# Performance work log

Hardware: AMD Instinct MI355X
Metric: run time of the kernel (lower is better)

The kernel has to match this reference:

```python
import jax, jax.numpy as jnp
import numpy as np

EPS = 1e-5
NUM_HEADS = 8
KEY_CH = 512
VAL_CH = 512


def instance_norm(x):
    # x: [B, N, C]; torch InstanceNorm1d normalizes over the length dim (N) per (b, c), no affine
    m = jnp.mean(x, axis=1, keepdims=True)
    v = jnp.var(x, axis=1, keepdims=True)
    return (x - m) / jnp.sqrt(v + EPS)


def setup_inputs() -> dict:
    key = jax.random.key(0)
    ks = jax.random.split(key, 16)
    B, HW, D, NL, LC = 8, 16384, 512, 20, 768
    s = 0.02
    inp = {
        "x": jax.random.normal(ks[0], (B, HW, D), dtype=jnp.float32),
        "l": jax.random.normal(ks[1], (B, NL, LC), dtype=jnp.float32),
        "l_mask": jnp.ones((B, NL), dtype=jnp.float32),
        # vis_project conv1d(dim->dim)
        "Wv": jax.random.normal(ks[2], (D, D), dtype=jnp.float32) * s,
        "bv": jnp.zeros((D,), dtype=jnp.float32),
        # f_query conv1d(v_in->key)
        "Wq": jax.random.normal(ks[3], (D, KEY_CH), dtype=jnp.float32) * s,
        "bq": jnp.zeros((KEY_CH,), dtype=jnp.float32),
        # f_key conv1d(l_in->key)
        "Wk": jax.random.normal(ks[4], (LC, KEY_CH), dtype=jnp.float32) * s,
        "bk": jnp.zeros((KEY_CH,), dtype=jnp.float32),
        # f_value conv1d(l_in->value)
        "Wval": jax.random.normal(ks[5], (LC, VAL_CH), dtype=jnp.float32) * s,
        "bval": jnp.zeros((VAL_CH,), dtype=jnp.float32),
        # W conv1d(value->out)
        "Ww": jax.random.normal(ks[6], (VAL_CH, VAL_CH), dtype=jnp.float32) * s,
        "bw": jnp.zeros((VAL_CH,), dtype=jnp.float32),
        # project_mm conv1d(value->value)
        "Wm": jax.random.normal(ks[7], (VAL_CH, VAL_CH), dtype=jnp.float32) * s,
        "bm": jnp.zeros((VAL_CH,), dtype=jnp.float32),
    }
    return inp


def reference(x, l, l_mask, Wv, bv, Wq, bq, Wk, bk, Wval, bval, Ww, bw, Wm, bm):
    B, HW, _ = x.shape
    n_l = l.shape[1]
    H = NUM_HEADS
    dk = KEY_CH // H
    dv = VAL_CH // H

    # vis_project: 1x1 conv + GELU (exact) + dropout(p=0)
    vis = jax.nn.gelu(x @ Wv + bv, approximate=False)  # [B, HW, D]

    # SpatialImageLanguageAttention
    q = instance_norm(x @ Wq + bq)          # [B, HW, Kc], InstanceNorm over HW
    k = l @ Wk + bk                          # [B, n_l, Kc]
    v = l @ Wval + bval                      # [B, n_l, Vc]

    q = q.reshape(B, HW, H, dk)              # bqhd
    k = k.reshape(B, n_l, H, dk)             # bkhd
    v = v.reshape(B, n_l, H, dv)             # bkhd

    sim = jnp.einsum("bqhd,bkhd->bhqk", q, k) * (KEY_CH ** -0.5)
    sim = jax.nn.softmax(sim, axis=-1)       # softmax over short language seq
    out = jnp.einsum("bhqk,bkhd->bqhd", sim, v).reshape(B, HW, VAL_CH)

    lang = instance_norm(out @ Ww + bw)      # [B, HW, Vc]

    # gated fusion + project_mm
    mm = vis * lang
    mm = jax.nn.gelu(mm @ Wm + bm, approximate=False)
    return mm
```

## Files before the change

### kernel.cpp

```cpp
#include <hip/hip_runtime.h>

#define HWN 16384
#define DMODEL 512
#define NLANG 20
#define LCH 768
#define NB 8
#define MTOT (NB*HWN)
#define NHEADS 8

typedef float floatx4 __attribute__((ext_vector_type(4)));
typedef short short8 __attribute__((ext_vector_type(8)));

__device__ __forceinline__ float bflo(unsigned u){ return __uint_as_float(u << 16); }
__device__ __forceinline__ float bfhi(unsigned u){ return __uint_as_float(u & 0xffff0000u); }
__device__ __forceinline__ unsigned short f2bf(float f){
  unsigned u = __float_as_uint(f);
  u += 0x7fffu + ((u >> 16) & 1u);
  return (unsigned short)(u >> 16);
}
__device__ __forceinline__ unsigned pack2(float a, float b){
  return (unsigned)f2bf(a) | ((unsigned)f2bf(b) << 16);
}
__device__ __forceinline__ float geluf(float v){
  float t = v * v;
  float u2 = v * fmaf(t, -0.0713548162f, -1.5957691216f);
  float e = __expf(u2);
  return v * __builtin_amdgcn_rcpf(1.0f + e);
}
__device__ __forceinline__ void stage16(const void* g, void* l){
  __builtin_amdgcn_global_load_lds(
      (const __attribute__((address_space(1))) void*)g,
      (__attribute__((address_space(3))) void*)l, 16, 0, 0);
}
__device__ __forceinline__ int tslot(int c){ return ((c & 7) << 3) | (c >> 3); }

template<int CTRL>
__device__ __forceinline__ float dppf(float x){
  return __int_as_float(__builtin_amdgcn_mov_dpp(__float_as_int(x), CTRL, 0xf, 0xf, true));
}
__device__ __forceinline__ void quadT(float v[4], int lane){
  float t0 = dppf<0xB1>(v[1]), t1 = dppf<0xB1>(v[0]);
  float t2 = dppf<0xB1>(v[3]), t3 = dppf<0xB1>(v[2]);
  int p0 = lane & 1;
  float w0 = (p0 == 0) ? v[0] : t0;
  float w1 = (p0 == 1) ? v[1] : t1;
  float w2 = (p0 == 0) ? v[2] : t2;
  float w3 = (p0 == 1) ? v[3] : t3;
  float s0 = dppf<0x4E>(w2), s1 = dppf<0x4E>(w3);
  float s2 = dppf<0x4E>(w0), s3 = dppf<0x4E>(w1);
  int p1 = lane & 2;
  v[0] = (p1 == 0) ? w0 : s0;
  v[1] = (p1 == 0) ? w1 : s1;
  v[2] = (p1 == 2) ? w2 : s2;
  v[3] = (p1 == 2) ? w3 : s3;
}

__global__ void prep_w(const float* __restrict__ Wv, const float* __restrict__ Wq,
                       const float* __restrict__ Wm,
                       unsigned short* __restrict__ wcatT, unsigned short* __restrict__ wmT)
{
  int i = blockIdx.x * 256 + threadIdx.x;
  if (i < 1024 * 512) {
    int n = i >> 9, k = i & 511;
    float v = (n < 512) ? Wv[k * 512 + n] : Wq[k * 512 + (n - 512)];
    wcatT[i] = f2bf(v);
  } else {
    int j = i - 1024 * 512;
    int n = j >> 9, k = j & 511;
    wmT[j] = f2bf(Wm[k * 512 + n]);
  }
}

__global__ void xcvt(const float* __restrict__ x, unsigned short* __restrict__ xb)
{
  size_t i = ((size_t)blockIdx.x * 256 + threadIdx.x) * 8;
  float4 a = *reinterpret_cast<const float4*>(&x[i]);
  float4 b = *reinterpret_cast<const float4*>(&x[i + 4]);
  uint4 d;
  d.x = pack2(a.x, a.y); d.y = pack2(a.z, a.w);
  d.z = pack2(b.x, b.y); d.w = pack2(b.z, b.w);
  *reinterpret_cast<uint4*>(&xb[i]) = d;
}

__global__ void mmk(const unsigned short* __restrict__ y, const unsigned short* __restrict__ vis,
                    const float* __restrict__ lma, const float* __restrict__ lmb,
                    unsigned short* __restrict__ mm)
{
  size_t i = ((size_t)blockIdx.x * 256 + threadIdx.x) * 8;
  int c = (int)(i & 511);
  int b = (int)(i >> 23);
  uint4 yv = *reinterpret_cast<const uint4*>(&y[i]);
  uint4 vv = *reinterpret_cast<const uint4*>(&vis[i]);
  const float* Ap = &lma[b * 512 + c];
  const float* Bp = &lmb[b * 512 + c];
  float4 a0 = *reinterpret_cast<const float4*>(Ap);
  float4 a1 = *reinterpret_cast<const float4*>(Ap + 4);
  float4 b0 = *reinterpret_cast<const float4*>(Bp);
  float4 b1 = *reinterpret_cast<const float4*>(Bp + 4);
  float m0 = bflo(vv.x) * (bflo(yv.x) * a0.x + b0.x);
  float m1 = bfhi(vv.x) * (bfhi(yv.x) * a0.y + b0.y);
  float m2 = bflo(vv.y) * (bflo(yv.y) * a0.z + b0.z);
  float m3 = bfhi(vv.y) * (bfhi(yv.y) * a0.w + b0.w);
  float m4 = bflo(vv.z) * (bflo(yv.z) * a1.x + b1.x);
  float m5 = bfhi(vv.z) * (bfhi(yv.z) * a1.y + b1.y);
  float m6 = bflo(vv.w) * (bflo(yv.w) * a1.z + b1.z);
  float m7 = bfhi(vv.w) * (bfhi(yv.w) * a1.w + b1.w);
  uint4 d;
  d.x = pack2(m0, m1); d.y = pack2(m2, m3);
  d.z = pack2(m4, m5); d.w = pack2(m6, m7);
  *reinterpret_cast<uint4*>(&mm[i]) = d;
}

__global__ void prep_kv(const float* __restrict__ l, const float* __restrict__ Wk,
                        const float* __restrict__ bk, const float* __restrict__ Wval,
                        const float* __restrict__ bval,
                        float* __restrict__ kraw, unsigned short* __restrict__ vb)
{
  int i = blockIdx.x * 256 + threadIdx.x;
  int which = i / (NB * NLANG * 512);
  int j = i - which * (NB * NLANG * 512);
  int bt = j >> 9;
  int c = j & 511;
  const float* W = which ? Wval : Wk;
  float acc = which ? bval[c] : bk[c];
  const float* lr = l + (size_t)bt * LCH;
  for (int p = 0; p < LCH; p++) acc = fmaf(lr[p], W[p * 512 + c], acc);
  if (which) vb[j] = f2bf(acc);
  else       kraw[j] = acc;
}

__global__ void w2prep(const unsigned short* __restrict__ vb, const float* __restrict__ Ww,
                       unsigned short* __restrict__ w2t)
{
  int i = blockIdx.x * 256 + threadIdx.x;
  int k = i & 255;
  int n = (i >> 8) & 511;
  int b = i >> 17;
  int t = k & 31, h = k >> 5;
  float acc = 0.f;
  if (t < NLANG) {
    const unsigned short* vr = &vb[(size_t)(b * NLANG + t) * 512 + h * 64];
    const float* wr = &Ww[(size_t)(h * 64) * 512 + n];
    #pragma unroll 8
    for (int d = 0; d < 64; d++)
      acc = fmaf(__uint_as_float((unsigned)vr[d] << 16), wr[d * 512], acc);
  }
  w2t[(size_t)(b * 512 + n) * 256 + k] = f2bf(acc);
}

__global__ void kprep(const float* __restrict__ qsum, const float* __restrict__ qsq,
                      const float* __restrict__ kraw, unsigned short* __restrict__ kp,
                      float* __restrict__ offG)
{
  int blk = blockIdx.x; int b = blk / NLANG, t = blk - b * NLANG;
  int lane = threadIdx.x;
  float offp = 0.f;
  float vals[8];
  #pragma unroll
  for (int e = 0; e < 8; e++) {
    int c = lane * 8 + e;
    float mean = qsum[b * 512 + c] * (1.f / 16384.f);
    float var  = qsq[b * 512 + c] * (1.f / 16384.f) - mean * mean;
    float inv  = rsqrtf(var + 1e-5f);
    float a = inv * 0.044194173824159216f;
    float kv = kraw[((size_t)(b * NLANG + t)) * 512 + c];
    vals[e] = kv * a;
    offp += (-mean * a) * kv;
  }
  unsigned u0 = pack2(vals[0], vals[1]);
  unsigned u1 = pack2(vals[2], vals[3]);
  unsigned u2 = pack2(vals[4], vals[5]);
  unsigned u3 = pack2(vals[6], vals[7]);
  uint4 uu = make_uint4(u0, u1, u2, u3);
  *reinterpret_cast<uint4*>(&kp[((size_t)(b * NLANG + t)) * 512 + tslot(lane) * 8]) = uu;
  offp += __shfl_xor(offp, 1);
  offp += __shfl_xor(offp, 2);
  offp += __shfl_xor(offp, 4);
  if ((lane & 7) == 0) offG[(b * 8 + (lane >> 3)) * NLANG + t] = offp;
}

__global__ void lmk(const float* __restrict__ ysum, const float* __restrict__ ysq,
                    float* __restrict__ lma, float* __restrict__ lmb)
{
  int i = blockIdx.x * 256 + threadIdx.x;
  if (i < NB * 512) {
    float mean = ysum[i] * (1.f / 16384.f);
    float var  = ysq[i] * (1.f / 16384.f) - mean * mean;
    float inv  = rsqrtf(var + 1e-5f);
    lma[i] = inv; lmb[i] = -mean * inv;
  }
}

__global__ __launch_bounds__(256, 3) void attn_k(
    const unsigned short* __restrict__ kp, const float* __restrict__ offG,
    const unsigned short* __restrict__ qb, unsigned short* __restrict__ pb)
{
  __shared__ __align__(16) unsigned short kps[NLANG * 512];
  __shared__ __align__(16) unsigned short qs[32 * 512];
  __shared__ float offs[NHEADS * NLANG];
  int tid = threadIdx.x, bid = blockIdx.x;
  int b = bid >> 9;
  int row0 = (bid & 511) * 32;
  size_t base = (size_t)b * (NLANG * 512);
  const uint4* kg = reinterpret_cast<const uint4*>(kp + base);
  uint4* kl = reinterpret_cast<uint4*>(kps);
  #pragma unroll
  for (int i = 0; i < 5; i++) { int o = i * 256 + tid; kl[o] = kg[o]; }
  if (tid < NHEADS * NLANG) offs[tid] = offG[b * (NHEADS * NLANG) + tid];

  size_t grow0 = (size_t)b * HWN + row0;
  #pragma unroll
  for (int i = 0; i < 8; i++) {
    int g = i * 256 + tid;
    int row = g >> 6, c = g & 63;
    uint4 d = *reinterpret_cast<const uint4*>(&qb[(grow0 + row) * 512 + c * 8]);
    *reinterpret_cast<uint4*>(&qs[row * 512 + tslot(c) * 8]) = d;
  }
  __syncthreads();

  int r = tid >> 3, h = tid & 7;
  float sim[NLANG];
  #pragma unroll
  for (int t = 0; t < NLANG; t++) sim[t] = offs[h * NLANG + t];
  #pragma unroll
  for (int j = 0; j < 8; j++) {
    uint4 qv = *reinterpret_cast<const uint4*>(&qs[r * 512 + (j * 8 + h) * 8]);
    float q0 = bflo(qv.x), q1 = bfhi(qv.x), q2 = bflo(qv.y), q3 = bfhi(qv.y);
    float q4 = bflo(qv.z), q5 = bfhi(qv.z), q6 = bflo(qv.w), q7 = bfhi(qv.w);
    #pragma unroll
    for (int t = 0; t < NLANG; t++) {
      uint4 kv = *reinterpret_cast<const uint4*>(&kps[t * 512 + (j * 8 + h) * 8]);
      float a = sim[t];
      a = fmaf(q0, bflo(kv.x), a); a = fmaf(q1, bfhi(kv.x), a);
      a = fmaf(q2, bflo(kv.y), a); a = fmaf(q3, bfhi(kv.y), a);
      a = fmaf(q4, bflo(kv.z), a); a = fmaf(q5, bfhi(kv.z), a);
      a = fmaf(q6, bflo(kv.w), a); a = fmaf(q7, bfhi(kv.w), a);
      sim[t] = a;
    }
  }
  float mx = sim[0];
  #pragma unroll
  for (int t = 1; t < NLANG; t++) mx = fmaxf(mx, sim[t]);
  float s = 0.f;
  #pragma unroll
  for (int t = 0; t < NLANG; t++) { float e = __expf(sim[t] - mx); sim[t] = e; s += e; }
  float invs = 1.f / s;
  #pragma unroll
  for (int t = 0; t < NLANG; t++) sim[t] *= invs;

  unsigned uu[16];
  #pragma unroll
  for (int j = 0; j < 10; j++) uu[j] = pack2(sim[2 * j], sim[2 * j + 1]);
  #pragma unroll
  for (int j = 10; j < 16; j++) uu[j] = 0u;
  size_t prow = (grow0 + r) * 256 + h * 32;
  #pragma unroll
  for (int j = 0; j < 4; j++)
    *reinterpret_cast<uint4*>(&pb[prow + j * 8]) =
        make_uint4(uu[4 * j], uu[4 * j + 1], uu[4 * j + 2], uu[4 * j + 3]);
}

template<int MODE, int KD>
__global__ __launch_bounds__(256) void gemm_k(
    const unsigned short* __restrict__ A,
    const unsigned short* __restrict__ Bw,
    const float* __restrict__ bias0, const float* __restrict__ bias1,
    unsigned short* __restrict__ Out0, unsigned short* __restrict__ Out1,
    float* __restrict__ OutF,
    float* __restrict__ sum1, float* __restrict__ sum2)
{
  constexpr int GN  = (MODE == 0) ? 8 : 4;
  constexpr int NWG = (MODE == 0) ? 8192 : 4096;
  constexpr int KT  = KD / 32;
  constexpr int CS  = 136;
  __shared__ __align__(16) unsigned short SM[6 * 128 * 32];

  int raw = blockIdx.x;
  int lid = (raw & 7) * (NWG / 8) + (raw >> 3);
  int tileN = lid & (GN - 1);
  int tileM = lid / GN;
  int tm128 = tileM * 128;
  int b512 = (tileM >> 7) * 512;
  int tid = threadIdx.x;
  int wave = tid >> 6, lane = tid & 63;
  int wr = (wave >> 1) * 64, wc = (wave & 1) * 64;
  int r15 = lane & 15, kcg = lane >> 4;

  floatx4 acc[4][4];
  floatx4 zz = {0.f, 0.f, 0.f, 0.f};
  #pragma unroll
  for (int m = 0; m < 4; m++)
    #pragma unroll
    for (int n = 0; n < 4; n++) acc[m][n] = zz;

  const unsigned short* Arow = A + (size_t)tm128 * KD;
  const unsigned short* Brow = Bw +
      ((MODE == 1) ? (size_t)(tileM >> 7) * 512 * KD : (size_t)0) +
      (size_t)(tileN * 128) * KD;

  auto stage = [&](int kt, int s) {
    int k0 = kt * 32;
    unsigned short* As = SM + s * 4096;
    unsigned short* Bs = SM + (3 + s) * 4096;
    #pragma unroll
    for (int i = 0; i < 2; i++) {
      int idx = i * 256 + tid;
      int row = idx >> 2;
      int c = (idx & 3) ^ ((row >> 1) & 3);
      stage16(&Arow[(size_t)row * KD + k0 + c * 8],
              &As[(i * 256 + wave * 64) * 8]);
    }
    #pragma unroll
    for (int i = 0; i < 2; i++) {
      int idx = i * 256 + tid;
      int row = idx >> 2;
      int c = (idx & 3) ^ ((row >> 1) & 3);
      stage16(&Brow[(size_t)row * KD + k0 + c * 8],
              &Bs[(i * 256 + wave * 64) * 8]);
    }
  };

  stage(0, 0);
  stage(1, 1);
  #pragma unroll
  for (int kt = 0; kt < KT; kt++) {
    int s = kt % 3;
    __builtin_amdgcn_sched_barrier(0);
    if (kt < KT - 1) asm volatile("s_waitcnt vmcnt(4) lgkmcnt(0)\n\ts_barrier" ::: "memory");
    else             asm volatile("s_waitcnt vmcnt(0) lgkmcnt(0)\n\ts_barrier" ::: "memory");
    __builtin_amdgcn_sched_barrier(0);
    if (kt + 2 < KT) stage(kt + 2, (kt + 2) % 3);
    const unsigned short* As = SM + s * 4096;
    const unsigned short* Bs = SM + (3 + s) * 4096;
    short8 af[4], bfv[4];
    #pragma unroll
    for (int m = 0; m < 4; m++) {
      int R = wr + m * 16 + r15;
      af[m] = *reinterpret_cast<const short8*>(&As[R * 32 + (kcg ^ ((R >> 1) & 3)) * 8]);
    }
    #pragma unroll
    for (int n = 0; n < 4; n++) {
      int R = wc + n * 16 + r15;
      bfv[n] = *reinterpret_cast<const short8*>(&Bs[R * 32 + (kcg ^ ((R >> 1) & 3)) * 8]);
    }
    #pragma unroll
    for (int m = 0; m < 4; m++)
      #pragma unroll
      for (int n = 0; n < 4; n++)
        acc[m][n] = __builtin_amdgcn_mfma_f32_16x16x32_bf16(af[m], bfv[n], acc[m][n], 0, 0, 0);
  }

  if constexpr (MODE != 2) __syncthreads();

  int rowTl = wr + (lane >> 4) * 4 + (lane & 3);
  int c4Tl  = wc + ((lane >> 2) & 3) * 4;

  if constexpr (MODE == 2) {
    #pragma unroll
    for (int n = 0; n < 4; n++) {
      int gcol = tileN * 128 + wc + n * 16 + r15;
      #pragma unroll
      for (int m = 0; m < 4; m++) {
        float v[4];
        #pragma unroll
        for (int j = 0; j < 4; j++) v[j] = geluf(acc[m][n][j] + bias0[gcol]);
        quadT(v, lane);
        int grow = tm128 + m * 16 + rowTl;
        int gc4  = tileN * 128 + n * 16 + c4Tl;
        float4 f4; f4.x = v[0]; f4.y = v[1]; f4.z = v[2]; f4.w = v[3];
        *reinterpret_cast<float4*>(&OutF[(size_t)grow * 512 + gc4]) = f4;
      }
    }
  } else {
    unsigned short* C = SM;
    #pragma unroll
    for (int n = 0; n < 4; n++) {
      int gcol = tileN * 128 + wc + n * 16 + r15;
      float s1 = 0.f, s2 = 0.f;
      #pragma unroll
      for (int m = 0; m < 4; m++) {
        float v[4];
        #pragma unroll
        for (int j = 0; j < 4; j++) v[j] = acc[m][n][j];
        if constexpr (MODE == 0) {
          if (tileN < 4) {
            #pragma unroll
            for (int j = 0; j < 4; j++) v[j] = geluf(v[j] + bias0[gcol]);
          } else {
            #pragma unroll
            for (int j = 0; j < 4; j++) { v[j] += bias1[gcol - 512]; s1 += v[j]; s2 += v[j] * v[j]; }
          }
        } else {
          #pragma unroll
          for (int j = 0; j < 4; j++) { v[j] += bias0[gcol]; s1 += v[j]; s2 += v[j] * v[j]; }
        }
        quadT(v, lane);
        int lrow = m * 16 + rowTl;
        int lc4  = n * 16 + c4Tl;
        uint2 d2; d2.x = pack2(v[0], v[1]); d2.y = pack2(v[2], v[3]);
        *reinterpret_cast<uint2*>(&C[lrow * CS + lc4]) = d2;
      }
      bool doStats = (MODE == 1) || (tileN >= 4);
      if (doStats) {
        s1 += __shfl_xor(s1, 16); s1 += __shfl_xor(s1, 32);
        s2 += __shfl_xor(s2, 16); s2 += __shfl_xor(s2, 32);
        if (lane < 16) {
          int c = (MODE == 0) ? (gcol - 512) : gcol;
          atomicAdd(&sum1[b512 + c], s1);
          atomicAdd(&sum2[b512 + c], s2);
        }
      }
    }
    __syncthreads();
    unsigned short* Og;
    int colbase;
    if constexpr (MODE == 0) {
      if (tileN < 4) { Og = Out0; colbase = tileN * 128; }
      else           { Og = Out1; colbase = (tileN - 4) * 128; }
    } else {
      Og = Out0; colbase = tileN * 128;
    }
    #pragma unroll
    for (int t = 0; t < 8; t++) {
      int cid = t * 256 + tid;
      int row = cid >> 4, cc = cid & 15;
      uint4 d = *reinterpret_cast<const uint4*>(&C[row * CS + cc * 8]);
      *reinterpret_cast<uint4*>(&Og[(size_t)(tm128 + row) * 512 + colbase + cc * 8]) = d;
    }
  }
}

extern "C" void kernel_launch(void* const* d_in, const int* in_sizes, int n_in,
                              void* d_out, int out_size, void* d_ws, size_t ws_size,
                              hipStream_t stream)
{
  const float* x   = (const float*)d_in[0];
  const float* l   = (const float*)d_in[1];
  const float* Wv  = (const float*)d_in[3];
  const float* bv  = (const float*)d_in[4];
  const float* Wq  = (const float*)d_in[5];
  const float* bq  = (const float*)d_in[6];
  const float* Wk  = (const float*)d_in[7];
  const float* bk  = (const float*)d_in[8];
  const float* Wva = (const float*)d_in[9];
  const float* bva = (const float*)d_in[10];
  const float* Ww  = (const float*)d_in[11];
  const float* bw  = (const float*)d_in[12];
  const float* Wm  = (const float*)d_in[13];
  const float* bm  = (const float*)d_in[14];

  char* w = (char*)d_ws;
  size_t o = 0;
  auto alloc = [&](size_t bytes) { size_t r = o; o += (bytes + 255) & ~(size_t)255; return r; };
  size_t WCATT = alloc(1024 * 512 * 2);
  size_t WMT   = alloc(512 * 512 * 2);
  size_t W2T   = alloc((size_t)NB * 512 * 256 * 2);
  size_t KRAW  = alloc((size_t)NB * NLANG * 512 * 4);
  size_t VB    = alloc((size_t)NB * NLANG * 512 * 2);
  size_t KP    = alloc((size_t)NB * NLANG * 512 * 2);
  size_t OFFW  = alloc((size_t)NB * NHEADS * NLANG * 4);
  size_t STATS = alloc((size_t)4 * NB * 512 * 4);
  size_t LMA   = alloc((size_t)NB * 512 * 4);
  size_t LMB   = alloc((size_t)NB * 512 * 4);
  size_t XB    = alloc((size_t)MTOT * 512 * 2);
  size_t VIS   = alloc((size_t)MTOT * 512 * 2);
  size_t QBUF  = alloc((size_t)MTOT * 512 * 2);
  size_t PB    = alloc((size_t)MTOT * 256 * 2);
  size_t YBUF  = alloc((size_t)MTOT * 512 * 2);

  float* qsum = (float*)(w + STATS);
  float* qsq  = qsum + NB * 512;
  float* ysum = qsq + NB * 512;
  float* ysq  = ysum + NB * 512;

  hipMemsetAsync(w + STATS, 0, (size_t)4 * NB * 512 * 4, stream);
  prep_w<<<3072, 256, 0, stream>>>(Wv, Wq, Wm,
      (unsigned short*)(w + WCATT), (unsigned short*)(w + WMT));
  xcvt<<<32768, 256, 0, stream>>>(x, (unsigned short*)(w + XB));
  prep_kv<<<640, 256, 0, stream>>>(l, Wk, bk, Wva, bva,
      (float*)(w + KRAW), (unsigned short*)(w + VB));
  w2prep<<<4096, 256, 0, stream>>>((const unsigned short*)(w + VB), Ww,
      (unsigned short*)(w + W2T));
  gemm_k<0, 512><<<8192, 256, 0, stream>>>((const unsigned short*)(w + XB),
      (const unsigned short*)(w + WCATT), bv, bq,
      (unsigned short*)(w + VIS), (unsigned short*)(w + QBUF), nullptr, qsum, qsq);
  kprep<<<160, 64, 0, stream>>>(qsum, qsq, (const float*)(w + KRAW),
      (unsigned short*)(w + KP), (float*)(w + OFFW));
  attn_k<<<4096, 256, 0, stream>>>((const unsigned short*)(w + KP),
      (const float*)(w + OFFW), (const unsigned short*)(w + QBUF),
      (unsigned short*)(w + PB));
  gemm_k<1, 256><<<4096, 256, 0, stream>>>((const unsigned short*)(w + PB),
      (const unsigned short*)(w + W2T), bw, nullptr,
      (unsigned short*)(w + YBUF), nullptr, nullptr, ysum, ysq);
  lmk<<<16, 256, 0, stream>>>(ysum, ysq, (float*)(w + LMA), (float*)(w + LMB));
  mmk<<<32768, 256, 0, stream>>>((const unsigned short*)(w + YBUF),
      (const unsigned short*)(w + VIS), (const float*)(w + LMA), (const float*)(w + LMB),
      (unsigned short*)(w + XB));
  gemm_k<2, 512><<<4096, 256, 0, stream>>>((const unsigned short*)(w + XB),
      (const unsigned short*)(w + WMT), bm, nullptr,
      nullptr, nullptr, (float*)d_out, nullptr, nullptr);
}
```

Measured before the change: 803.3 us.

## Fuse fp32->bf16 conversion and gating multiply into GEMM A-operand staging

Removes the standalone xcvt and mmk elementwise kernels. The first GEMM now loads fp32 x through registers and converts it to bf16 before writing LDS. The last GEMM reads Y and VIS directly and applies the instance-norm affine and gating multiply while staging its A tile. This saves several full-size HBM round trips, around a gigabyte of traffic, at the cost of register-staged A loads and extra VGPR pressure in the GEMM pipeline. Each block also redundantly re-reads A across its N tiles.

```diff
diff --git a/kernel.cpp b/kernel.cpp
--- a/kernel.cpp
+++ b/kernel.cpp
@@ -71,46 +71,6 @@
   }
 }
 
-__global__ void xcvt(const float* __restrict__ x, unsigned short* __restrict__ xb)
-{
-  size_t i = ((size_t)blockIdx.x * 256 + threadIdx.x) * 8;
-  float4 a = *reinterpret_cast<const float4*>(&x[i]);
-  float4 b = *reinterpret_cast<const float4*>(&x[i + 4]);
-  uint4 d;
-  d.x = pack2(a.x, a.y); d.y = pack2(a.z, a.w);
-  d.z = pack2(b.x, b.y); d.w = pack2(b.z, b.w);
-  *reinterpret_cast<uint4*>(&xb[i]) = d;
-}
-
-__global__ void mmk(const unsigned short* __restrict__ y, const unsigned short* __restrict__ vis,
-                    const float* __restrict__ lma, const float* __restrict__ lmb,
-                    unsigned short* __restrict__ mm)
-{
-  size_t i = ((size_t)blockIdx.x * 256 + threadIdx.x) * 8;
-  int c = (int)(i & 511);
-  int b = (int)(i >> 23);
-  uint4 yv = *reinterpret_cast<const uint4*>(&y[i]);
-  uint4 vv = *reinterpret_cast<const uint4*>(&vis[i]);
-  const float* Ap = &lma[b * 512 + c];
-  const float* Bp = &lmb[b * 512 + c];
-  float4 a0 = *reinterpret_cast<const float4*>(Ap);
-  float4 a1 = *reinterpret_cast<const float4*>(Ap + 4);
-  float4 b0 = *reinterpret_cast<const float4*>(Bp);
-  float4 b1 = *reinterpret_cast<const float4*>(Bp + 4);
-  float m0 = bflo(vv.x) * (bflo(yv.x) * a0.x + b0.x);
-  float m1 = bfhi(vv.x) * (bfhi(yv.x) * a0.y + b0.y);
-  float m2 = bflo(vv.y) * (bflo(yv.y) * a0.z + b0.z);
-  float m3 = bfhi(vv.y) * (bfhi(yv.y) * a0.w + b0.w);
-  float m4 = bflo(vv.z) * (bflo(yv.z) * a1.x + b1.x);
-  float m5 = bfhi(vv.z) * (bfhi(yv.z) * a1.y + b1.y);
-  float m6 = bflo(vv.w) * (bflo(yv.w) * a1.z + b1.z);
-  float m7 = bfhi(vv.w) * (bfhi(yv.w) * a1.w + b1.w);
-  uint4 d;
-  d.x = pack2(m0, m1); d.y = pack2(m2, m3);
-  d.z = pack2(m4, m5); d.w = pack2(m6, m7);
-  *reinterpret_cast<uint4*>(&mm[i]) = d;
-}
-
 __global__ void prep_kv(const float* __restrict__ l, const float* __restrict__ Wk,
                         const float* __restrict__ bk, const float* __restrict__ Wval,
                         const float* __restrict__ bval,
@@ -262,7 +222,9 @@
 
 template<int MODE, int KD>
 __global__ __launch_bounds__(256) void gemm_k(
-    const unsigned short* __restrict__ A,
+    const void* __restrict__ Ag,
+    const unsigned short* __restrict__ Vis,
+    const float* __restrict__ lmA, const float* __restrict__ lmB,
     const unsigned short* __restrict__ Bw,
     const float* __restrict__ bias0, const float* __restrict__ bias1,
     unsigned short* __restrict__ Out0, unsigned short* __restrict__ Out1,
@@ -273,7 +235,9 @@
   constexpr int NWG = (MODE == 0) ? 8192 : 4096;
   constexpr int KT  = KD / 32;
   constexpr int CS  = 136;
-  __shared__ __align__(16) unsigned short SM[6 * 128 * 32];
+  constexpr bool REGA = (MODE != 1);
+  __shared__ __align__(16) unsigned short SM[6 * 4096 + 2048];
+  float* CO = reinterpret_cast<float*>(SM + 6 * 4096);
 
   int raw = blockIdx.x;
   int lid = (raw & 7) * (NWG / 8) + (raw >> 3);
@@ -293,43 +257,122 @@
     #pragma unroll
     for (int n = 0; n < 4; n++) acc[m][n] = zz;
 
-  const unsigned short* Arow = A + (size_t)tm128 * KD;
+  const float* ArowF = nullptr;
+  const unsigned short* ArowS = nullptr;
+  const unsigned short* VisRow = nullptr;
+  if constexpr (MODE == 0) ArowF = (const float*)Ag + (size_t)tm128 * 512;
+  else                     ArowS = (const unsigned short*)Ag + (size_t)tm128 * KD;
+  if constexpr (MODE == 2) VisRow = Vis + (size_t)tm128 * 512;
   const unsigned short* Brow = Bw +
       ((MODE == 1) ? (size_t)(tileM >> 7) * 512 * KD : (size_t)0) +
       (size_t)(tileN * 128) * KD;
 
-  auto stage = [&](int kt, int s) {
-    int k0 = kt * 32;
-    unsigned short* As = SM + s * 4096;
-    unsigned short* Bs = SM + (3 + s) * 4096;
+  float4 rF[2][4];
+  uint4  rY[2][2], rV[2][2];
+
+  auto stageB = [&](int kt) {
+    unsigned short* Bs = SM + (3 + kt % 3) * 4096;
     #pragma unroll
     for (int i = 0; i < 2; i++) {
       int idx = i * 256 + tid;
       int row = idx >> 2;
       int c = (idx & 3) ^ ((row >> 1) & 3);
-      stage16(&Arow[(size_t)row * KD + k0 + c * 8],
-              &As[(i * 256 + wave * 64) * 8]);
-    }
+      stage16(&Brow[(size_t)row * KD + kt * 32 + c * 8], &Bs[(i * 256 + wave * 64) * 8]);
+    }
+  };
+  auto stageAg = [&](int kt) {
+    unsigned short* As = SM + (kt % 3) * 4096;
     #pragma unroll
     for (int i = 0; i < 2; i++) {
       int idx = i * 256 + tid;
       int row = idx >> 2;
       int c = (idx & 3) ^ ((row >> 1) & 3);
-      stage16(&Brow[(size_t)row * KD + k0 + c * 8],
-              &Bs[(i * 256 + wave * 64) * 8]);
+      stage16(&ArowS[(size_t)row * KD + kt * 32 + c * 8], &As[(i * 256 + wave * 64) * 8]);
     }
   };
-
-  stage(0, 0);
-  stage(1, 1);
+  auto stageLoad = [&](int kt, int ph) {
+    #pragma unroll
+    for (int i = 0; i < 2; i++) {
+      int idx = i * 256 + tid;
+      int row = idx >> 2;
+      int c = (idx & 3) ^ ((row >> 1) & 3);
+      if constexpr (MODE == 0) {
+        const float* p = &ArowF[(size_t)row * 512 + kt * 32 + c * 8];
+        rF[ph][2 * i]     = *reinterpret_cast<const float4*>(p);
+        rF[ph][2 * i + 1] = *reinterpret_cast<const float4*>(p + 4);
+      } else {
+        size_t ga = (size_t)row * 512 + kt * 32 + c * 8;
+        rY[ph][i] = *reinterpret_cast<const uint4*>(&ArowS[ga]);
+        rV[ph][i] = *reinterpret_cast<const uint4*>(&VisRow[ga]);
+      }
+    }
+  };
+  auto stageWrite = [&](int kt, int ph) {
+    unsigned short* As = SM + (kt % 3) * 4096;
+    #pragma unroll
+    for (int i = 0; i < 2; i++) {
+      int idx = i * 256 + tid;
+      uint4 d;
+      if constexpr (MODE == 0) {
+        float4 a = rF[ph][2 * i], b = rF[ph][2 * i + 1];
+        d.x = pack2(a.x, a.y); d.y = pack2(a.z, a.w);
+        d.z = pack2(b.x, b.y); d.w = pack2(b.z, b.w);
+      } else {
+        int row = idx >> 2;
+        int c = (idx & 3) ^ ((row >> 1) & 3);
+        int k = kt * 32 + c * 8;
+        float4 a0 = *reinterpret_cast<const float4*>(&CO[k]);
+        float4 a1 = *reinterpret_cast<const float4*>(&CO[k + 4]);
+        float4 c0 = *reinterpret_cast<const float4*>(&CO[512 + k]);
+        float4 c1 = *reinterpret_cast<const float4*>(&CO[512 + k + 4]);
+        uint4 yv = rY[ph][i], vv = rV[ph][i];
+        float m0 = bflo(vv.x) * (bflo(yv.x) * a0.x + c0.x);
+        float m1 = bfhi(vv.x) * (bfhi(yv.x) * a0.y + c0.y);
+        float m2 = bflo(vv.y) * (bflo(yv.y) * a0.z + c0.z);
+        float m3 = bfhi(vv.y) * (bfhi(yv.y) * a0.w + c0.w);
+        float m4 = bflo(vv.z) * (bflo(yv.z) * a1.x + c1.x);
+        float m5 = bfhi(vv.z) * (bfhi(yv.z) * a1.y + c1.y);
+        float m6 = bflo(vv.w) * (bflo(yv.w) * a1.z + c1.z);
+        float m7 = bfhi(vv.w) * (bfhi(yv.w) * a1.w + c1.w);
+        d.x = pack2(m0, m1); d.y = pack2(m2, m3);
+        d.z = pack2(m4, m5); d.w = pack2(m6, m7);
+      }
+      *reinterpret_cast<uint4*>(&As[idx * 8]) = d;
+    }
+  };
+
+  if constexpr (MODE == 2) {
+    float4 v = (tid < 128) ? *reinterpret_cast<const float4*>(&lmA[b512 + tid * 4])
+                           : *reinterpret_cast<const float4*>(&lmB[b512 + (tid - 128) * 4]);
+    *reinterpret_cast<float4*>(&CO[tid * 4]) = v;
+    __syncthreads();
+  }
+
+  if constexpr (REGA) {
+    stageLoad(0, 0); stageB(0);
+    stageLoad(1, 1); stageB(1);
+    stageWrite(0, 0);
+  } else {
+    stageAg(0); stageB(0);
+    stageAg(1); stageB(1);
+  }
   #pragma unroll
   for (int kt = 0; kt < KT; kt++) {
     int s = kt % 3;
     __builtin_amdgcn_sched_barrier(0);
-    if (kt < KT - 1) asm volatile("s_waitcnt vmcnt(4) lgkmcnt(0)\n\ts_barrier" ::: "memory");
-    else             asm volatile("s_waitcnt vmcnt(0) lgkmcnt(0)\n\ts_barrier" ::: "memory");
+    if (kt < KT - 1) {
+      if constexpr (REGA) asm volatile("s_waitcnt vmcnt(6) lgkmcnt(0)\n\ts_barrier" ::: "memory");
+      else                asm volatile("s_waitcnt vmcnt(4) lgkmcnt(0)\n\ts_barrier" ::: "memory");
+    } else {
+      asm volatile("s_waitcnt vmcnt(0) lgkmcnt(0)\n\ts_barrier" ::: "memory");
+    }
     __builtin_amdgcn_sched_barrier(0);
-    if (kt + 2 < KT) stage(kt + 2, (kt + 2) % 3);
+    if constexpr (REGA) {
+      if (kt + 2 < KT) { stageLoad(kt + 2, kt & 1); stageB(kt + 2); }
+      if (kt + 1 < KT) stageWrite(kt + 1, (kt + 1) & 1);
+    } else {
+      if (kt + 2 < KT) { stageAg(kt + 2); stageB(kt + 2); }
+    }
     const unsigned short* As = SM + s * 4096;
     const unsigned short* Bs = SM + (3 + s) * 4096;
     short8 af[4], bfv[4];
@@ -462,7 +505,6 @@
   size_t STATS = alloc((size_t)4 * NB * 512 * 4);
   size_t LMA   = alloc((size_t)NB * 512 * 4);
   size_t LMB   = alloc((size_t)NB * 512 * 4);
-  size_t XB    = alloc((size_t)MTOT * 512 * 2);
   size_t VIS   = alloc((size_t)MTOT * 512 * 2);
   size_t QBUF  = alloc((size_t)MTOT * 512 * 2);
   size_t PB    = alloc((size_t)MTOT * 256 * 2);
@@ -476,12 +518,11 @@
   hipMemsetAsync(w + STATS, 0, (size_t)4 * NB * 512 * 4, stream);
   prep_w<<<3072, 256, 0, stream>>>(Wv, Wq, Wm,
       (unsigned short*)(w + WCATT), (unsigned short*)(w + WMT));
-  xcvt<<<32768, 256, 0, stream>>>(x, (unsigned short*)(w + XB));
   prep_kv<<<640, 256, 0, stream>>>(l, Wk, bk, Wva, bva,
       (float*)(w + KRAW), (unsigned short*)(w + VB));
   w2prep<<<4096, 256, 0, stream>>>((const unsigned short*)(w + VB), Ww,
       (unsigned short*)(w + W2T));
-  gemm_k<0, 512><<<8192, 256, 0, stream>>>((const unsigned short*)(w + XB),
+  gemm_k<0, 512><<<8192, 256, 0, stream>>>(x, nullptr, nullptr, nullptr,
       (const unsigned short*)(w + WCATT), bv, bq,
       (unsigned short*)(w + VIS), (unsigned short*)(w + QBUF), nullptr, qsum, qsq);
   kprep<<<160, 64, 0, stream>>>(qsum, qsq, (const float*)(w + KRAW),
@@ -489,14 +530,12 @@
   attn_k<<<4096, 256, 0, stream>>>((const unsigned short*)(w + KP),
       (const float*)(w + OFFW), (const unsigned short*)(w + QBUF),
       (unsigned short*)(w + PB));
-  gemm_k<1, 256><<<4096, 256, 0, stream>>>((const unsigned short*)(w + PB),
+  gemm_k<1, 256><<<4096, 256, 0, stream>>>((const void*)(w + PB), nullptr, nullptr, nullptr,
       (const unsigned short*)(w + W2T), bw, nullptr,
       (unsigned short*)(w + YBUF), nullptr, nullptr, ysum, ysq);
   lmk<<<16, 256, 0, stream>>>(ysum, ysq, (float*)(w + LMA), (float*)(w + LMB));
-  mmk<<<32768, 256, 0, stream>>>((const unsigned short*)(w + YBUF),
+  gemm_k<2, 512><<<4096, 256, 0, stream>>>((const void*)(w + YBUF),
       (const unsigned short*)(w + VIS), (const float*)(w + LMA), (const float*)(w + LMB),
-      (unsigned short*)(w + XB));
-  gemm_k<2, 512><<<4096, 256, 0, stream>>>((const unsigned short*)(w + XB),
       (const unsigned short*)(w + WMT), bm, nullptr,
       nullptr, nullptr, (float*)d_out, nullptr, nullptr);
 }
```

Result: slower. 1.044 ms (+29.9%).
